# Performance work log

Measured on AMD Instinct MI355X. Metric: run time of the kernel, lower is better.

Reference implementation:

```python
import jax, jax.numpy as jnp
import numpy as np

E = 8        # num_experts
K = 2        # top_k
B, S, D, H = 4, 2048, 1024, 2048  # batch, seq, input_size, hidden_size (GLU -> 2H fan-out)


def act_quant(x):
    # per-token 8-bit absmax quantization (BitNet style)
    scale = 127.0 / jnp.clip(jnp.max(jnp.abs(x), axis=-1, keepdims=True), 1e-5)
    return jnp.clip(jnp.round(x * scale), -128, 127) / scale


def weight_quant(w):
    # per-(expert)-tensor 1.58-bit quantization to {-1,0,1}/scale
    scale = 1.0 / jnp.clip(jnp.mean(jnp.abs(w)), 1e-5)
    return jnp.clip(jnp.round(w * scale), -1, 1) / scale


def ste(x, q):
    # straight-through estimator: forward uses q, backward passes grad of x
    return x + jax.lax.stop_gradient(q - x)


def setup_inputs() -> dict:
    key = jax.random.key(0)
    k0, k1, k2, k3 = jax.random.split(key, 4)
    x = jax.random.normal(k0, (B, S, D), jnp.float32)
    w_gate = jax.random.normal(k1, (D, E), jnp.float32) * 0.02   # router (no bias)
    w_in = jax.random.normal(k2, (E, 2 * H, D), jnp.float32) * 0.02   # ParallelExperts1_58b input_linear [E, out, in]
    w_out = jax.random.normal(k3, (E, D, H), jnp.float32) * 0.02      # output_linear [E, out, in]
    bias = jnp.zeros((D,), jnp.float32)
    return {"x": x, "w_gate": w_gate, "w_in": w_in, "w_out": w_out, "bias": bias}


def reference(x, w_gate, w_in, w_out, bias):
    bsz, length, d = x.shape
    xf = x.reshape(-1, d)                               # [N, D]
    logits = xf @ w_gate                                # [N, E]
    top_logits, top_idx = jax.lax.top_k(logits, K)      # [N, K]
    gates = jax.nn.softmax(top_logits, axis=-1)         # [N, K]

    # load-balancing aux loss (switch loss + z-loss), training-mode router loss
    probs = jax.nn.softmax(logits, axis=-1)
    onehot = jax.nn.one_hot(top_idx, E, dtype=logits.dtype).sum(axis=1)  # [N, E]
    freq = onehot.sum(axis=0)
    p = probs.sum(axis=0)
    switchloss = E * jnp.sum((p / jnp.sum(p)) * (freq / jnp.sum(freq)))
    zloss = jnp.sum(jax.nn.logsumexp(logits, axis=-1) ** 2) / xf.shape[0]
    loss = switchloss + 0.1 * zloss

    # STE-quantized activations and per-expert ternary weights
    xq = ste(xf, act_quant(xf))                          # [N, D]
    win_q = jax.vmap(lambda w: ste(w, weight_quant(w)))(w_in)    # [E, 2H, D]
    wout_q = jax.vmap(lambda w: ste(w, weight_quant(w)))(w_out)  # [E, D, H]

    # dense expert loop (E is small/static); gates zero-out non-routed tokens,
    # equivalent to the gather/grouped-GEMM/index_add pipeline in the original.
    y = jnp.zeros_like(xf)
    for e in range(E):
        gate_e = jnp.sum(jnp.where(top_idx == e, gates, 0.0), axis=1)  # [N]
        h = xq @ win_q[e].T                              # [N, 2H]
        h1, g = jnp.split(h, 2, axis=-1)
        h = jax.nn.silu(h1) * g                          # GLU
        hq = ste(h, act_quant(h))
        y = y + gate_e[:, None] * (hq @ wout_q[e].T)     # [N, D]

    y = y.reshape(bsz, length, d) + bias
    return y, loss
```

## Files before the change

kernel.cpp:

```cpp
#include <hip/hip_runtime.h>
#include <math.h>

typedef __attribute__((ext_vector_type(4)))  int   i32x4;
typedef __attribute__((ext_vector_type(16))) int   i32x16;
typedef __attribute__((ext_vector_type(4)))  float f32x4;
typedef __attribute__((ext_vector_type(8)))  unsigned short u16x8;

#define NTOK   8192
#define DIMD   1024
#define HID    2048
#define NEXP   8
#define NPAIR  16384

#define XQ_OFF      0L
#define WQIN_OFF    8388608L
#define WQOUT_OFF   41943040L
#define XG_OFF      58720256L
#define HG_OFF      79691776L
#define GLUG_OFF    121634816L
#define XRECG_OFF   205520896L
#define GATE_OFF    205602816L
#define HRECG_OFF   205668352L
#define TLIST_OFF   205750272L
#define CNT_OFF     206012416L
#define PSUM_OFF    206012448L
#define ZSUM_OFF    206012480L
#define PART_OFF    206012512L
#define WRECIN_OFF  206015616L
#define WRECOUT_OFF 206015648L
#define WSCLIN_OFF  206015680L
#define WSCLOUT_OFF 206015712L
#define OFF_OFF     206015744L

__device__ __forceinline__ int clampi(int v, int lo, int hi){ return v<lo?lo:(v>hi?hi:v); }

__device__ __forceinline__ unsigned packq(f32x4 v, float s, int lo, int hi){
  int q0 = clampi((int)rintf(v.x*s), lo, hi);
  int q1 = clampi((int)rintf(v.y*s), lo, hi);
  int q2 = clampi((int)rintf(v.z*s), lo, hi);
  int q3 = clampi((int)rintf(v.w*s), lo, hi);
  return (unsigned)((q0&255)|((q1&255)<<8)|((q2&255)<<16)|((q3&255)<<24));
}

__device__ __forceinline__ unsigned short f2bf(float f){
  unsigned u = __float_as_uint(f);
  u += 0x7fffu + ((u >> 16) & 1u);
  return (unsigned short)(u >> 16);
}
__device__ __forceinline__ float bf2f(unsigned short b){
  return __uint_as_float(((unsigned)b) << 16);
}

__global__ void k_init(int* __restrict__ cnts, float* __restrict__ psum, float* __restrict__ zsum){
  int i = threadIdx.x;
  if (i < 8){ cnts[i]=0; psum[i]=0.f; }
  if (i == 8) zsum[0]=0.f;
}

__global__ __launch_bounds__(1024) void k_router(
    const float* __restrict__ x, const float* __restrict__ wg,
    signed char* __restrict__ xq, float* __restrict__ xrec,
    float* __restrict__ gatep, int* __restrict__ tlist, int* __restrict__ cnts,
    float* __restrict__ psum, float* __restrict__ zsum)
{
  __shared__ float ls_p[8]; __shared__ float ls_z[1];
  __shared__ int ls_c[8];  __shared__ int ls_b[8];
  int tid = threadIdx.x;
  if (tid<8){ ls_p[tid]=0.f; ls_c[tid]=0; }
  if (tid==8) ls_z[0]=0.f;
  __syncthreads();
  int wave = tid>>6, lane = tid&63;
  int tok = blockIdx.x*16 + wave;

  const f32x4* x4 = (const f32x4*)(x + (long)tok*DIMD) + lane*4;
  f32x4 xv[4];
  #pragma unroll
  for (int j=0;j<4;++j) xv[j] = x4[j];

  float amax = 0.f;
  float lg[8] = {0,0,0,0,0,0,0,0};
  const f32x4* wg4 = (const f32x4*)wg;
  #pragma unroll
  for (int j=0;j<16;++j){
    float xd = xv[j>>2][j&3];
    amax = fmaxf(amax, fabsf(xd));
    int d = lane*16 + j;
    f32x4 w0 = wg4[d*2], w1 = wg4[d*2+1];
    lg[0]+=xd*w0.x; lg[1]+=xd*w0.y; lg[2]+=xd*w0.z; lg[3]+=xd*w0.w;
    lg[4]+=xd*w1.x; lg[5]+=xd*w1.y; lg[6]+=xd*w1.z; lg[7]+=xd*w1.w;
  }
  for (int m=1;m<64;m<<=1){
    amax = fmaxf(amax, __shfl_xor(amax, m));
    #pragma unroll
    for (int e=0;e<8;++e) lg[e] += __shfl_xor(lg[e], m);
  }
  float cm = fmaxf(amax, 1e-5f);
  float sx = 127.f/cm;
  unsigned p0 = packq(xv[0], sx, -128, 127);
  unsigned p1 = packq(xv[1], sx, -128, 127);
  unsigned p2 = packq(xv[2], sx, -128, 127);
  unsigned p3 = packq(xv[3], sx, -128, 127);
  i32x4 pk; pk.x=(int)p0; pk.y=(int)p1; pk.z=(int)p2; pk.w=(int)p3;
  *(i32x4*)(xq + (long)tok*DIMD + lane*16) = pk;

  int e1=0, e2=0, s1=0, s2=0;
  if (lane==0){
    xrec[tok] = cm*(1.f/127.f);
    e1 = 0;
    for (int e=1;e<8;++e) if (lg[e] > lg[e1]) e1 = e;
    e2 = (e1==0)?1:0;
    for (int e=0;e<8;++e) if (e!=e1 && lg[e] > lg[e2]) e2 = e;
    float t = expf(lg[e2]-lg[e1]);
    gatep[tok*2]   = 1.f/(1.f+t);
    gatep[tok*2+1] = t/(1.f+t);
    float mx = lg[e1], sum = 0.f, pr[8];
    #pragma unroll
    for (int e=0;e<8;++e){ pr[e] = expf(lg[e]-mx); sum += pr[e]; }
    float inv = 1.f/sum;
    #pragma unroll
    for (int e=0;e<8;++e) atomicAdd(&ls_p[e], pr[e]*inv);
    float lse = mx + logf(sum);
    atomicAdd(&ls_z[0], lse*lse);
    s1 = atomicAdd(&ls_c[e1], 1);
    s2 = atomicAdd(&ls_c[e2], 1);
  }
  __syncthreads();
  if (tid<8) ls_b[tid] = atomicAdd(&cnts[tid], ls_c[tid]);
  __syncthreads();
  if (lane==0){
    tlist[e1*NTOK + ls_b[e1] + s1] = tok*2;
    tlist[e2*NTOK + ls_b[e2] + s2] = tok*2 + 1;
  }
  if (tid<8)  atomicAdd(&psum[tid], ls_p[tid]);
  if (tid==8) atomicAdd(zsum, ls_z[0]);
}

__global__ void k_wabs(const float* __restrict__ w_in, const float* __restrict__ w_out,
                       float* __restrict__ part){
  int b = blockIdx.x, tid = threadIdx.x;
  const float* base = (b < 512) ? (w_in + (long)b*65536) : (w_out + (long)(b-512)*65536);
  const f32x4* p4 = (const f32x4*)base;
  float s = 0.f;
  for (int i = tid; i < 16384; i += 256){
    f32x4 v = p4[i];
    s += fabsf(v.x)+fabsf(v.y)+fabsf(v.z)+fabsf(v.w);
  }
  __shared__ float red[256];
  red[tid] = s; __syncthreads();
  for (int off=128; off; off>>=1){ if (tid<off) red[tid]+=red[tid+off]; __syncthreads(); }
  if (tid==0) part[b] = red[0];
}

__global__ void k_wmean(const float* __restrict__ part, const int* __restrict__ cnts,
                        float* __restrict__ wrec_in, float* __restrict__ wrec_out,
                        float* __restrict__ wscl_in, float* __restrict__ wscl_out,
                        int* __restrict__ off){
  int t = threadIdx.x;
  if (t < 8){
    float s = 0.f;
    for (int i=0;i<64;++i) s += part[t*64+i];
    float cmm = fmaxf(s/4194304.f, 1e-5f);
    wrec_in[t] = cmm; wscl_in[t] = 1.f/cmm;
  } else if (t < 16){
    int e = t-8; float s = 0.f;
    for (int i=0;i<32;++i) s += part[512 + e*32 + i];
    float cmm = fmaxf(s/2097152.f, 1e-5f);
    wrec_out[e] = cmm; wscl_out[e] = 1.f/cmm;
  } else if (t == 16){
    int acc = 0;
    for (int e=0;e<8;++e){ off[e] = acc; acc += (cnts[e] + 511) & ~511; }
  }
}

__global__ void k_packw(const float* __restrict__ w, i32x4* __restrict__ wq,
                        const float* __restrict__ wscl, int COLS, int K, int KB,
                        long chunksPerE){
  long t = (long)blockIdx.x*blockDim.x + threadIdx.x;
  int e = (int)(t / chunksPerE);
  long r = t - (long)e*chunksPerE;
  int lane = (int)(r & 63);
  long fb = r >> 6;
  int kb = (int)(fb % KB);
  int cb = (int)(fb / KB);
  int col = cb*32 + (lane & 31);
  int k0  = kb*32 + (lane >> 5)*16;
  const f32x4* src = (const f32x4*)(w + ((long)e*COLS + col)*K + k0);
  float s = wscl[e];
  f32x4 v0 = src[0], v1 = src[1], v2 = src[2], v3 = src[3];
  i32x4 o;
  o.x = (int)packq(v0, s, -1, 1);
  o.y = (int)packq(v1, s, -1, 1);
  o.z = (int)packq(v2, s, -1, 1);
  o.w = (int)packq(v3, s, -1, 1);
  wq[t] = o;
}

__global__ void k_gatherx(const signed char* __restrict__ xq, const int* __restrict__ tlist,
                          const int* __restrict__ cnts, const int* __restrict__ off,
                          const float* __restrict__ xrec,
                          signed char* __restrict__ xg, float* __restrict__ xrecg){
  int e = blockIdx.x & 7;
  int cnt = cnts[e];
  int w = threadIdx.x >> 6;
  int c = threadIdx.x & 63;
  int goff = off[e];
  signed char* xb = xg + (long)goff*1024;
  for (int r = (blockIdx.x>>3)*4 + w; r < cnt; r += 2048){
    int pr = tlist[e*NTOK + r];
    if (c == 0) xrecg[goff + r] = xrec[pr>>1];
    i32x4 v = *(const i32x4*)(xq + (long)(pr>>1)*DIMD + c*16);
    int kb = c>>1, lhi = c&1;
    *(i32x4*)(xb + ((long)(r>>5)*32 + kb)*1024 + (lhi*32 + (r&31))*16) = v;
  }
}

#define MF(A,B,C) C = __builtin_amdgcn_mfma_i32_32x32x32_i8(A,B,C,0,0,0)

__global__ __launch_bounds__(512, 4) void k_gemm1(
    const signed char* __restrict__ xg, const signed char* __restrict__ wqin,
    const int* __restrict__ cnts, const int* __restrict__ off,
    const float* __restrict__ xrecg_all, const float* __restrict__ wrec_in,
    unsigned short* __restrict__ glug_all)
{
  __shared__ signed char bsh[65536];
  const int e = blockIdx.x & 7;
  const int ctile = blockIdx.x >> 3;
  const int cnt = cnts[e];
  const int tid = threadIdx.x;
  const int goff = off[e];
  {
    const i32x4* s0 = (const i32x4*)(wqin + (long)e*4194304 + (long)ctile*32768);
    const i32x4* s1 = (const i32x4*)(wqin + (long)e*4194304 + (long)(64+ctile)*32768);
    i32x4* d = (i32x4*)bsh;
    #pragma unroll
    for (int i=0;i<4;++i){ d[tid + i*512] = s0[tid + i*512]; d[2048 + tid + i*512] = s1[tid + i*512]; }
  }
  __syncthreads();

  const int wave = tid>>6, lane = tid&63, l31 = lane&31, lhi = lane>>5;
  const float wr = wrec_in[e];
  const float* xrecg = xrecg_all + goff;
  unsigned short* glug = glug_all + (long)goff*HID;
  const signed char* xbase = xg + (long)goff*1024;
  const signed char* lb = bsh + lane*16;
  const int maxit = (cnt + 511) >> 9;

  #pragma unroll 1
  for (int it=0; it<maxit; ++it){
    const int rb = it*512 + wave*64;
    const i32x4* a0 = (const i32x4*)(xbase + (long)(rb>>5)*32768) + lane;
    const i32x4* a1 = a0 + 2048;

    i32x16 p0=(i32x16)0, p1=(i32x16)0, q0=(i32x16)0, q1=(i32x16)0;
    i32x4 eA0=a0[0], eA1=a1[0];
    i32x4 oA0=a0[64], oA1=a1[64];
    i32x4 eB0=*(const i32x4*)(lb),      eB1=*(const i32x4*)(lb+32768);
    i32x4 oB0=*(const i32x4*)(lb+1024), oB1=*(const i32x4*)(lb+33792);
    #pragma unroll 1
    for (int kb=0; kb<30; kb+=2){
      a0+=128; a1+=128;
      MF(eA0,eB0,p0); MF(eA1,eB0,p1); MF(eA0,eB1,q0); MF(eA1,eB1,q1);
      eA0=a0[0]; eA1=a1[0];
      eB0=*(const i32x4*)(lb + (kb+2)*1024);
      eB1=*(const i32x4*)(lb + 32768 + (kb+2)*1024);
      MF(oA0,oB0,p0); MF(oA1,oB0,p1); MF(oA0,oB1,q0); MF(oA1,oB1,q1);
      oA0=a0[64]; oA1=a1[64];
      oB0=*(const i32x4*)(lb + (kb+3)*1024);
      oB1=*(const i32x4*)(lb + 32768 + (kb+3)*1024);
    }
    MF(eA0,eB0,p0); MF(eA1,eB0,p1); MF(eA0,eB1,q0); MF(eA1,eB1,q1);
    MF(oA0,oB0,p0); MF(oA1,oB0,p1); MF(oA0,oB1,q0); MF(oA1,oB1,q1);

#define GLUEPI(P,Q,ROFF) { \
    _Pragma("unroll") \
    for (int g=0; g<16; ++g){ \
      int r = rb + ROFF + (g&3) + 8*(g>>2) + 4*lhi; \
      if (r < cnt){ \
        float dq = xrecg[r]*wr; \
        float h1 = (float)P[g]*dq; \
        float gg = (float)Q[g]*dq; \
        float v = h1/(1.f+expf(-h1))*gg; \
        glug[(long)r*HID + ctile*32 + l31] = f2bf(v); \
      } \
    } }
    GLUEPI(p0,q0,0)
    GLUEPI(p1,q1,32)
#undef GLUEPI
  }
}

__global__ __launch_bounds__(256) void k_quanthg(
    const unsigned short* __restrict__ glug, const int* __restrict__ tlist,
    const int* __restrict__ cnts, const int* __restrict__ off,
    const float* __restrict__ gatep, signed char* __restrict__ hg, float* __restrict__ hrecg){
  __shared__ float wmax[4];
  int e = blockIdx.x & 7;
  int cnt = cnts[e];
  const int* tl = tlist + e*NTOK;
  int goff = off[e];
  const int c = threadIdx.x;
  const int wv = c>>6, lane = c&63;
  signed char* hb = hg + (long)goff*2048;
  for (int r = blockIdx.x>>3; r < cnt; r += 2048){
    u16x8 v = *(const u16x8*)(glug + (long)(goff+r)*HID + c*8);
    float f0=bf2f(v[0]), f1=bf2f(v[1]), f2=bf2f(v[2]), f3=bf2f(v[3]);
    float f4=bf2f(v[4]), f5=bf2f(v[5]), f6=bf2f(v[6]), f7=bf2f(v[7]);
    float m = fmaxf(fmaxf(fmaxf(fabsf(f0),fabsf(f1)),fmaxf(fabsf(f2),fabsf(f3))),
                    fmaxf(fmaxf(fabsf(f4),fabsf(f5)),fmaxf(fabsf(f6),fabsf(f7))));
    #pragma unroll
    for (int mm=1; mm<64; mm<<=1) m = fmaxf(m, __shfl_xor(m, mm));
    if (lane==0) wmax[wv] = m;
    __syncthreads();
    float am = fmaxf(fmaxf(wmax[0],wmax[1]), fmaxf(wmax[2],wmax[3]));
    float cmm = fmaxf(am, 1e-5f);
    if (c == 0) hrecg[goff + r] = gatep[tl[r]] * cmm * (1.f/127.f);
    float s = 127.f/cmm;
    f32x4 a, b;
    a.x=f0; a.y=f1; a.z=f2; a.w=f3; b.x=f4; b.y=f5; b.z=f6; b.w=f7;
    uint2 u; u.x = packq(a, s, -128, 127); u.y = packq(b, s, -128, 127);
    int kb = c>>2, lhi = (c>>1)&1, h = c&1;
    *(uint2*)(hb + ((long)(r>>5)*64 + kb)*1024 + (lhi*32 + (r&31))*16 + h*8) = u;
    __syncthreads();
  }
}

__global__ __launch_bounds__(512, 4) void k_gemm2(
    const signed char* __restrict__ hg, const signed char* __restrict__ wqout,
    const int* __restrict__ tlist, const int* __restrict__ cnts, const int* __restrict__ off,
    const float* __restrict__ hrecg_all, const float* __restrict__ wrec_out,
    float* __restrict__ pout)
{
  __shared__ signed char bsh[65536];
  const int e = blockIdx.x & 7;
  const int j = blockIdx.x >> 3;
  const int ctile = j & 31;
  const int rh = j >> 5;
  const int cnt = cnts[e];
  const int tid = threadIdx.x;
  const int goff = off[e];
  {
    const i32x4* s0 = (const i32x4*)(wqout + (long)e*2097152 + (long)ctile*65536);
    i32x4* d = (i32x4*)bsh;
    #pragma unroll
    for (int i=0;i<8;++i) d[tid + i*512] = s0[tid + i*512];
  }
  __syncthreads();

  const int wave = tid>>6, lane = tid&63, l31 = lane&31, lhi = lane>>5;
  const int* tl = tlist + e*NTOK;
  const float wr = wrec_out[e];
  const float* hrecg = hrecg_all + goff;
  const signed char* hbase = hg + (long)goff*2048;
  const signed char* lb = bsh + lane*16;
  const int maxit = (cnt + 1023) >> 10;

  #pragma unroll 1
  for (int it=rh; it<maxit; it+=2){
    const int rb = it*1024 + wave*128;
    const i32x4* a0 = (const i32x4*)(hbase + (long)(rb>>5)*65536) + lane;
    const i32x4* a1 = a0 + 4096;
    const i32x4* a2 = a0 + 8192;
    const i32x4* a3 = a0 + 12288;

    i32x16 c0=(i32x16)0, c1=(i32x16)0, c2=(i32x16)0, c3=(i32x16)0;
    i32x4 eA0=a0[0], eA1=a1[0], eA2=a2[0], eA3=a3[0];
    i32x4 oA0=a0[64], oA1=a1[64], oA2=a2[64], oA3=a3[64];
    i32x4 eB=*(const i32x4*)(lb);
    i32x4 oB=*(const i32x4*)(lb+1024);
    #pragma unroll 1
    for (int kb=0; kb<62; kb+=2){
      a0+=128; a1+=128; a2+=128; a3+=128;
      MF(eA0,eB,c0); MF(eA1,eB,c1); MF(eA2,eB,c2); MF(eA3,eB,c3);
      eA0=a0[0]; eA1=a1[0]; eA2=a2[0]; eA3=a3[0];
      eB=*(const i32x4*)(lb + (kb+2)*1024);
      MF(oA0,oB,c0); MF(oA1,oB,c1); MF(oA2,oB,c2); MF(oA3,oB,c3);
      oA0=a0[64]; oA1=a1[64]; oA2=a2[64]; oA3=a3[64];
      oB=*(const i32x4*)(lb + (kb+3)*1024);
    }
    MF(eA0,eB,c0); MF(eA1,eB,c1); MF(eA2,eB,c2); MF(eA3,eB,c3);
    MF(oA0,oB,c0); MF(oA1,oB,c1); MF(oA2,oB,c2); MF(oA3,oB,c3);

#define OUTEPI(C,ROFF) { \
    _Pragma("unroll") \
    for (int g=0; g<16; ++g){ \
      int r = rb + ROFF + (g&3) + 8*(g>>2) + 4*lhi; \
      if (r < cnt){ \
        int pr = tl[r]; \
        float f = hrecg[r]*wr; \
        pout[(long)pr*DIMD + ctile*32 + l31] = (float)C[g]*f; \
      } \
    } }
    OUTEPI(c0,0)
    OUTEPI(c1,32)
    OUTEPI(c2,64)
    OUTEPI(c3,96)
#undef OUTEPI
  }
}

__global__ void k_combine(const float* __restrict__ pout, const float* __restrict__ bias,
                          float* __restrict__ y){
  long idx = (long)blockIdx.x*blockDim.x + threadIdx.x;
  int tok = (int)(idx >> 8);
  int c4  = (int)(idx & 255);
  f32x4 b  = ((const f32x4*)bias)[c4];
  const f32x4* p = (const f32x4*)(pout + (long)tok*2*DIMD);
  f32x4 r = b + p[c4] + p[256 + c4];
  ((f32x4*)(y + (long)tok*DIMD))[c4] = r;
}

__global__ void k_loss(const int* __restrict__ cnts, const float* __restrict__ psum,
                       const float* __restrict__ zsum, float* __restrict__ out){
  if (threadIdx.x==0 && blockIdx.x==0){
    float sp=0.f, sf=0.f, sw=0.f;
    for (int e=0;e<8;++e){
      float f = (float)cnts[e];
      sp += psum[e]; sf += f; sw += psum[e]*f;
    }
    float loss = 8.f*sw/(sp*sf) + 0.1f*zsum[0]/(float)NTOK;
    out[(long)NTOK*DIMD] = loss;
  }
}

extern "C" void kernel_launch(void* const* d_in, const int* in_sizes, int n_in,
                              void* d_out, int out_size, void* d_ws, size_t ws_size,
                              hipStream_t stream){
  const float* x     = (const float*)d_in[0];
  const float* wg    = (const float*)d_in[1];
  const float* w_in  = (const float*)d_in[2];
  const float* w_out = (const float*)d_in[3];
  const float* bias  = (const float*)d_in[4];
  float* y = (float*)d_out;
  char* ws = (char*)d_ws;

  signed char* xq    = (signed char*)(ws + XQ_OFF);
  signed char* wqin  = (signed char*)(ws + WQIN_OFF);
  signed char* wqout = (signed char*)(ws + WQOUT_OFF);
  signed char* xg    = (signed char*)(ws + XG_OFF);
  signed char* hg    = (signed char*)(ws + HG_OFF);
  unsigned short* glug = (unsigned short*)(ws + GLUG_OFF);
  float* pout  = (float*)(ws + GLUG_OFF);
  float* xrecg = (float*)(ws + XRECG_OFF);
  float* gatep = (float*)(ws + GATE_OFF);
  float* hrecg = (float*)(ws + HRECG_OFF);
  int* tlist = (int*)(ws + TLIST_OFF);
  int* cnts  = (int*)(ws + CNT_OFF);
  float* psum = (float*)(ws + PSUM_OFF);
  float* zsum = (float*)(ws + ZSUM_OFF);
  float* part = (float*)(ws + PART_OFF);
  float* wrec_in  = (float*)(ws + WRECIN_OFF);
  float* wrec_out = (float*)(ws + WRECOUT_OFF);
  float* wscl_in  = (float*)(ws + WSCLIN_OFF);
  float* wscl_out = (float*)(ws + WSCLOUT_OFF);
  int* offe = (int*)(ws + OFF_OFF);

  float* xrec = (float*)(ws + XRECG_OFF);
  xrec = (float*)(ws + HRECG_OFF);

  k_init  <<<1, 64, 0, stream>>>(cnts, psum, zsum);
  k_router<<<512, 1024, 0, stream>>>(x, wg, xq, xrec, gatep, tlist, cnts, psum, zsum);
  k_wabs  <<<768, 256, 0, stream>>>(w_in, w_out, part);
  k_wmean <<<1, 64, 0, stream>>>(part, cnts, wrec_in, wrec_out, wscl_in, wscl_out, offe);
  k_packw <<<8192, 256, 0, stream>>>(w_in,  (i32x4*)wqin,  wscl_in,  4096, 1024, 32, 262144L);
  k_packw <<<4096, 256, 0, stream>>>(w_out, (i32x4*)wqout, wscl_out, 1024, 2048, 64, 131072L);
  k_gatherx<<<4096, 256, 0, stream>>>(xq, tlist, cnts, offe, xrec, xg, xrecg);
  k_gemm1 <<<512, 512, 0, stream>>>(xg, wqin, cnts, offe, xrecg, wrec_in, glug);
  k_quanthg<<<16384, 256, 0, stream>>>(glug, tlist, cnts, offe, gatep, hg, hrecg);
  k_gemm2 <<<512, 512, 0, stream>>>(hg, wqout, tlist, cnts, offe, hrecg, wrec_out, pout);
  k_combine<<<8192, 256, 0, stream>>>(pout, bias, y);
  k_loss  <<<1, 64, 0, stream>>>(cnts, psum, zsum, y);
}
```

Baseline: 407.9 us.

## Restructure GLU-quant kernel per-wave, add MFMA setprio, cheaper GLU epilogue

k_quanthg now gives each wave one row, loading the full row into registers and reducing the absmax with shuffles only. This drops the shared-memory max, the block barriers and the strided row loop. Both GEMM kernels wrap their MFMA groups in s_setprio so matrix issue is favored over loads from co-resident waves. The GEMM1 epilogue loads the per-row scale once per lane and broadcasts it with __shfl, and uses fast exp plus a hardware reciprocal in place of the IEEE division, which slightly changes numerics. The xrecg read for lanes past cnt may touch padding or neighbouring workspace, and the launch grid of 16384 blocks must still cover every row at four rows per block.

```diff
diff --git a/kernel.cpp b/kernel.cpp
--- a/kernel.cpp
+++ b/kernel.cpp
@@ -248,6 +248,7 @@
   #pragma unroll 1
   for (int it=0; it<maxit; ++it){
     const int rb = it*512 + wave*64;
+    const float xr = xrecg[rb + lane];
     const i32x4* a0 = (const i32x4*)(xbase + (long)(rb>>5)*32768) + lane;
     const i32x4* a1 = a0 + 2048;
 
@@ -259,29 +260,35 @@
     #pragma unroll 1
     for (int kb=0; kb<30; kb+=2){
       a0+=128; a1+=128;
+      __builtin_amdgcn_s_setprio(1);
       MF(eA0,eB0,p0); MF(eA1,eB0,p1); MF(eA0,eB1,q0); MF(eA1,eB1,q1);
+      __builtin_amdgcn_s_setprio(0);
       eA0=a0[0]; eA1=a1[0];
       eB0=*(const i32x4*)(lb + (kb+2)*1024);
       eB1=*(const i32x4*)(lb + 32768 + (kb+2)*1024);
+      __builtin_amdgcn_s_setprio(1);
       MF(oA0,oB0,p0); MF(oA1,oB0,p1); MF(oA0,oB1,q0); MF(oA1,oB1,q1);
+      __builtin_amdgcn_s_setprio(0);
       oA0=a0[64]; oA1=a1[64];
       oB0=*(const i32x4*)(lb + (kb+3)*1024);
       oB1=*(const i32x4*)(lb + 32768 + (kb+3)*1024);
     }
+    __builtin_amdgcn_s_setprio(1);
     MF(eA0,eB0,p0); MF(eA1,eB0,p1); MF(eA0,eB1,q0); MF(eA1,eB1,q1);
     MF(oA0,oB0,p0); MF(oA1,oB0,p1); MF(oA0,oB1,q0); MF(oA1,oB1,q1);
+    __builtin_amdgcn_s_setprio(0);
 
 #define GLUEPI(P,Q,ROFF) { \
     _Pragma("unroll") \
     for (int g=0; g<16; ++g){ \
-      int r = rb + ROFF + (g&3) + 8*(g>>2) + 4*lhi; \
-      if (r < cnt){ \
-        float dq = xrecg[r]*wr; \
-        float h1 = (float)P[g]*dq; \
-        float gg = (float)Q[g]*dq; \
-        float v = h1/(1.f+expf(-h1))*gg; \
-        glug[(long)r*HID + ctile*32 + l31] = f2bf(v); \
-      } \
+      int rl = ROFF + (g&3) + 8*(g>>2) + 4*lhi; \
+      int r = rb + rl; \
+      float dq = __shfl(xr, rl)*wr; \
+      float h1 = (float)P[g]*dq; \
+      float gg = (float)Q[g]*dq; \
+      float t = __expf(-h1); \
+      float v = h1*gg*__builtin_amdgcn_rcpf(1.f+t); \
+      if (r < cnt) glug[(long)r*HID + ctile*32 + l31] = f2bf(v); \
     } }
     GLUEPI(p0,q0,0)
     GLUEPI(p1,q1,32)
@@ -293,35 +300,46 @@
     const unsigned short* __restrict__ glug, const int* __restrict__ tlist,
     const int* __restrict__ cnts, const int* __restrict__ off,
     const float* __restrict__ gatep, signed char* __restrict__ hg, float* __restrict__ hrecg){
-  __shared__ float wmax[4];
   int e = blockIdx.x & 7;
   int cnt = cnts[e];
+  const int wv = threadIdx.x>>6, lane = threadIdx.x&63;
+  int r = (blockIdx.x>>3)*4 + wv;
+  if (r >= cnt) return;
   const int* tl = tlist + e*NTOK;
   int goff = off[e];
-  const int c = threadIdx.x;
-  const int wv = c>>6, lane = c&63;
   signed char* hb = hg + (long)goff*2048;
-  for (int r = blockIdx.x>>3; r < cnt; r += 2048){
-    u16x8 v = *(const u16x8*)(glug + (long)(goff+r)*HID + c*8);
-    float f0=bf2f(v[0]), f1=bf2f(v[1]), f2=bf2f(v[2]), f3=bf2f(v[3]);
-    float f4=bf2f(v[4]), f5=bf2f(v[5]), f6=bf2f(v[6]), f7=bf2f(v[7]);
-    float m = fmaxf(fmaxf(fmaxf(fabsf(f0),fabsf(f1)),fmaxf(fabsf(f2),fabsf(f3))),
-                    fmaxf(fmaxf(fabsf(f4),fabsf(f5)),fmaxf(fabsf(f6),fabsf(f7))));
-    #pragma unroll
-    for (int mm=1; mm<64; mm<<=1) m = fmaxf(m, __shfl_xor(m, mm));
-    if (lane==0) wmax[wv] = m;
-    __syncthreads();
-    float am = fmaxf(fmaxf(wmax[0],wmax[1]), fmaxf(wmax[2],wmax[3]));
-    float cmm = fmaxf(am, 1e-5f);
-    if (c == 0) hrecg[goff + r] = gatep[tl[r]] * cmm * (1.f/127.f);
-    float s = 127.f/cmm;
-    f32x4 a, b;
-    a.x=f0; a.y=f1; a.z=f2; a.w=f3; b.x=f4; b.y=f5; b.z=f6; b.w=f7;
-    uint2 u; u.x = packq(a, s, -128, 127); u.y = packq(b, s, -128, 127);
-    int kb = c>>2, lhi = (c>>1)&1, h = c&1;
-    *(uint2*)(hb + ((long)(r>>5)*64 + kb)*1024 + (lhi*32 + (r&31))*16 + h*8) = u;
-    __syncthreads();
-  }
+  const unsigned short* row = glug + (long)(goff+r)*HID;
+
+  u16x8 v0 = *(const u16x8*)(row + lane*8);
+  u16x8 v1 = *(const u16x8*)(row + 512 + lane*8);
+  u16x8 v2 = *(const u16x8*)(row + 1024 + lane*8);
+  u16x8 v3 = *(const u16x8*)(row + 1536 + lane*8);
+  float m = 0.f;
+  #pragma unroll
+  for (int j=0;j<8;++j){
+    m = fmaxf(m, fmaxf(fmaxf(fabsf(bf2f(v0[j])), fabsf(bf2f(v1[j]))),
+                       fmaxf(fabsf(bf2f(v2[j])), fabsf(bf2f(v3[j])))));
+  }
+  #pragma unroll
+  for (int mm=1; mm<64; mm<<=1) m = fmaxf(m, __shfl_xor(m, mm));
+  float cmm = fmaxf(m, 1e-5f);
+  if (lane == 0) hrecg[goff + r] = gatep[tl[r]] * cmm * (1.f/127.f);
+  float s = 127.f/cmm;
+
+#define QCHUNK(V, CIDX) { \
+    f32x4 a, b; \
+    a.x=bf2f(V[0]); a.y=bf2f(V[1]); a.z=bf2f(V[2]); a.w=bf2f(V[3]); \
+    b.x=bf2f(V[4]); b.y=bf2f(V[5]); b.z=bf2f(V[6]); b.w=bf2f(V[7]); \
+    uint2 u; u.x = packq(a, s, -128, 127); u.y = packq(b, s, -128, 127); \
+    int c = (CIDX); \
+    int kb = c>>2, lhi = (c>>1)&1, h = c&1; \
+    *(uint2*)(hb + ((long)(r>>5)*64 + kb)*1024 + (lhi*32 + (r&31))*16 + h*8) = u; \
+  }
+  QCHUNK(v0, lane)
+  QCHUNK(v1, lane+64)
+  QCHUNK(v2, lane+128)
+  QCHUNK(v3, lane+192)
+#undef QCHUNK
 }
 
 __global__ __launch_bounds__(512, 4) void k_gemm2(
@@ -370,15 +388,21 @@
     #pragma unroll 1
     for (int kb=0; kb<62; kb+=2){
       a0+=128; a1+=128; a2+=128; a3+=128;
+      __builtin_amdgcn_s_setprio(1);
       MF(eA0,eB,c0); MF(eA1,eB,c1); MF(eA2,eB,c2); MF(eA3,eB,c3);
+      __builtin_amdgcn_s_setprio(0);
       eA0=a0[0]; eA1=a1[0]; eA2=a2[0]; eA3=a3[0];
       eB=*(const i32x4*)(lb + (kb+2)*1024);
+      __builtin_amdgcn_s_setprio(1);
       MF(oA0,oB,c0); MF(oA1,oB,c1); MF(oA2,oB,c2); MF(oA3,oB,c3);
+      __builtin_amdgcn_s_setprio(0);
       oA0=a0[64]; oA1=a1[64]; oA2=a2[64]; oA3=a3[64];
       oB=*(const i32x4*)(lb + (kb+3)*1024);
     }
+    __builtin_amdgcn_s_setprio(1);
     MF(eA0,eB,c0); MF(eA1,eB,c1); MF(eA2,eB,c2); MF(eA3,eB,c3);
     MF(oA0,oB,c0); MF(oA1,oB,c1); MF(oA2,oB,c2); MF(oA3,oB,c3);
+    __builtin_amdgcn_s_setprio(0);
 
 #define OUTEPI(C,ROFF) { \
     _Pragma("unroll") \
@@ -454,8 +478,7 @@
   float* wscl_out = (float*)(ws + WSCLOUT_OFF);
   int* offe = (int*)(ws + OFF_OFF);
 
-  float* xrec = (float*)(ws + XRECG_OFF);
-  xrec = (float*)(ws + HRECG_OFF);
+  float* xrec = (float*)(ws + HRECG_OFF);
 
   k_init  <<<1, 64, 0, stream>>>(cnts, psum, zsum);
   k_router<<<512, 1024, 0, stream>>>(x, wg, xq, xrec, gatep, tlist, cnts, psum, zsum);
```

New measurement: 420.8 us. 1.03x slower.
